# Kernel tuning notes

Hardware: AMD Instinct MI355X
Metric: run time of the kernel (lower is better)

The kernel has to match this reference:

```python
import jax, jax.numpy as jnp
import numpy as np


def setup_inputs() -> dict:
    key = jax.random.key(0)
    B, D, F = 8192, 768, 32768
    k_x, k_w = jax.random.split(key, 2)
    x = jax.random.normal(k_x, (B, D), dtype=jnp.float32)
    # xavier_normal init for W_enc: std = sqrt(2/(fan_in+fan_out))
    scale = (2.0 / (D + F)) ** 0.5
    W_enc = jax.random.normal(k_w, (D, F), dtype=jnp.float32) * scale
    # W_dec = W_enc.T with unit-norm rows (latent directions)
    W_dec = W_enc.T
    W_dec = W_dec / jnp.linalg.norm(W_dec, axis=1, keepdims=True)
    pre_bias = jnp.zeros((D,), dtype=jnp.float32)
    latent_bias = jnp.zeros((F,), dtype=jnp.float32)
    return {"x": x, "pre_bias": pre_bias, "W_enc": W_enc,
            "latent_bias": latent_bias, "W_dec": W_dec, "k": 32}


def reference(x, pre_bias, W_enc, latent_bias, W_dec, k):
    # encode: [B,F]
    latents_pre_act = (x - pre_bias) @ W_enc + latent_bias
    # topk selection then relu: relu(topk(pre_act, k))
    vals, idx = jax.lax.top_k(latents_pre_act, k)      # [B,k]
    vals = jax.nn.relu(vals)
    # sparse decode: gather only the k selected decoder rows per example
    # W_dec[idx]: [B,k,D]
    recons = jnp.einsum('bk,bkd->bd', vals, W_dec[idx]) + pre_bias
    return recons
```

## Files before the change

### kernel.cpp

```cpp
#include <hip/hip_runtime.h>
#include <stdint.h>

#define GAS __attribute__((address_space(1)))
#define LAS __attribute__((address_space(3)))

typedef __attribute__((ext_vector_type(4))) float f32x4;
typedef unsigned char uchar;
typedef long long i64f;

static constexpr int NB = 8192;
static constexpr int DD = 768;
static constexpr int FF = 32768;
static constexpr int TK = 32;
static constexpr int RUNC = 64;
static constexpr int SLOT = 8;
static constexpr int NSEG = FF / 128;
static constexpr int SORTN = 1024;
static constexpr int NS2 = 256;
static constexpr int NKT = DD / 32;
static constexpr int PQ8 = 128 * 32;
static constexpr float WSC = 64.0f;
static constexpr float WSCI = 1.0f / 64.0f;

__device__ __forceinline__ ushort f2bf(float f) {
    unsigned x = __float_as_uint(f);
    unsigned r = (x + 0x7FFFu + ((x >> 16) & 1u)) >> 16;
    return (ushort)r;
}
__device__ __forceinline__ ushort sortkey(ushort u) {
    return (u & 0x8000u) ? (ushort)(u ^ 0xFFFFu) : (ushort)(u | 0x8000u);
}
__device__ __forceinline__ float e4m3f(uchar b) {
    int e = (b >> 3) & 0xF, m = b & 7;
    float v = (e == 0) ? ldexpf((float)m, -9) : ldexpf((float)(8 + m), e - 10);
    return (b & 0x80) ? -v : v;
}
__device__ __forceinline__ uchar f2e4m3(float v) {
    return (uchar)(__builtin_amdgcn_cvt_pk_fp8_f32(v, v, 0, false) & 0xFF);
}
__device__ __forceinline__ void gload_lds16(const void* g, void* l) {
    __builtin_amdgcn_global_load_lds((const GAS unsigned int*)g,
                                     (LAS unsigned int*)l, 16, 0, 0);
}
__device__ __forceinline__ size_t pan_off8(int v, int d) {
    return ((size_t)(v >> 7) * NKT + (d >> 5)) * PQ8 + ((v & 127) << 5) + (d & 31);
}

__global__ __launch_bounds__(256) void prep_x_k(const float* __restrict__ x,
                                                const float* __restrict__ pb,
                                                uchar* __restrict__ Ap) {
    const int n4 = NB * DD / 4;
    for (int i = blockIdx.x * 256 + threadIdx.x; i < n4; i += gridDim.x * 256) {
        int b = i / (DD / 4), dq = (i % (DD / 4)) * 4;
        float4 v = ((const float4*)x)[i];
        float4 p = ((const float4*)pb)[i % (DD / 4)];
        int w = __builtin_amdgcn_cvt_pk_fp8_f32(v.x - p.x, v.y - p.y, 0, false);
        w = __builtin_amdgcn_cvt_pk_fp8_f32(v.z - p.z, v.w - p.w, w, true);
        *(unsigned*)(Ap + pan_off8(b, dq)) = (unsigned)w;
    }
}

__global__ __launch_bounds__(256) void prep_w_k(const float* __restrict__ W,
                                                uchar* __restrict__ Bp,
                                                float* __restrict__ Wt32,
                                                float* __restrict__ s2part) {
    __shared__ float tile[32][33];
    int f0 = blockIdx.x * 32, d0 = blockIdx.y * 32;
    int tx = threadIdx.x & 31, ty = threadIdx.x >> 5;
    float ss = 0.f;
#pragma unroll
    for (int q = 0; q < 4; q++) {
        int dl = ty + q * 8;
        float v = W[(size_t)(d0 + dl) * FF + f0 + tx];
        tile[dl][tx] = v;
        ss += v * v;
    }
#pragma unroll
    for (int o = 32; o >= 1; o >>= 1) ss += __shfl_down(ss, o);
    if ((threadIdx.x & 63) == 0) {
        int slot = (blockIdx.x * 97 + blockIdx.y * 13 + (threadIdx.x >> 6)) & (NS2 - 1);
        atomicAdd(&s2part[slot], ss);
    }
    __syncthreads();
#pragma unroll
    for (int q = 0; q < 4; q++) {
        int fl = ty + q * 8;
        float v = tile[tx][fl];
        int f = f0 + fl, d = d0 + tx;
        Bp[pan_off8(f, d)] = f2e4m3(v * WSC);
        if (Wt32) Wt32[(size_t)f * DD + d] = v;
    }
}

__global__ __launch_bounds__(256) void rn_k(const float* __restrict__ x,
                                            const float* __restrict__ pb,
                                            const float* __restrict__ s2part,
                                            float* __restrict__ tau) {
    int t = threadIdx.x, l = t & 63, w = t >> 6;
    __shared__ float wsum[4];
    __shared__ float s2m;
    float p = s2part[t];
#pragma unroll
    for (int o = 32; o >= 1; o >>= 1) p += __shfl_down(p, o);
    if (l == 0) wsum[w] = p;
    __syncthreads();
    if (t == 0) s2m = (wsum[0] + wsum[1] + wsum[2] + wsum[3]) / ((float)DD * (float)FF);
    __syncthreads();
    int row = blockIdx.x * 4 + w;
    float ss = 0.f;
#pragma unroll
    for (int q = 0; q < 12; q++) {
        int d = l + 64 * q;
        float v = x[(size_t)row * DD + d] - pb[d];
        ss += v * v;
    }
#pragma unroll
    for (int o = 32; o >= 1; o >>= 1) ss += __shfl_down(ss, o);
    if (l == 0) tau[row] = 2.75f * sqrtf(s2m * ss);
}

__global__ __launch_bounds__(256, 3) void gemm_k(const uchar* __restrict__ Ap,
                                                 const uchar* __restrict__ Bp,
                                                 const float* __restrict__ lbias,
                                                 const float* __restrict__ tau,
                                                 unsigned* __restrict__ cand,
                                                 unsigned* __restrict__ rowbad) {
    __shared__ __align__(16) char smem[24576];

    int bid = (int)blockIdx.x;
    int wg = (bid & 7) * 2048 + (bid >> 3);
    int mt = wg >> 8, nt = wg & 255;
    int m0 = mt << 7, n0 = nt << 7;

    int t = threadIdx.x, l = t & 63, w = t >> 6;
    int wm = w >> 1, wn = w & 1;

    int so = ((t >> 1) << 5) + (((t & 1) ^ ((t >> 3) & 1)) << 4);
    const uchar* sA = Ap + (size_t)mt * NKT * PQ8 + so;
    const uchar* sB = Bp + (size_t)nt * NKT * PQ8 + so;

    int sw = ((l >> 2) & 1) << 1;
    int aro = ((wm << 6) + (l & 15)) * 32 + (((l >> 4) ^ sw) << 3);
    int bro = ((wn << 6) + (l & 15)) * 32 + (((l >> 4) ^ sw) << 3);

    f32x4 acc[4][4] = {};

#define STAGE(slot, kt)                                                       \
    {                                                                         \
        const size_t o = (size_t)(kt) * PQ8;                                  \
        char* base = smem + (slot) * 8192;                                    \
        gload_lds16(sA + o, base + t * 16);                                   \
        gload_lds16(sB + o, base + 4096 + t * 16);                            \
    }

    STAGE(0, 0)
    STAGE(1, 1)
    asm volatile("s_waitcnt vmcnt(2)" ::: "memory");
    __builtin_amdgcn_s_barrier();
    __builtin_amdgcn_sched_barrier(0);

    int cur = 0;
#pragma unroll 1
    for (int kt = 0; kt < NKT; kt++) {
        const char* As = smem + cur * 8192;
        const char* Bs = As + 4096;
        int nxt = cur + 2; if (nxt >= 3) nxt -= 3;
        if (kt < NKT - 2) STAGE(nxt, kt + 2)

        i64f af[4], bfr[4];
        af[0]  = *(const i64f*)(As + aro);
        af[1]  = *(const i64f*)(As + aro + 512);
        af[2]  = *(const i64f*)(As + aro + 1024);
        af[3]  = *(const i64f*)(As + aro + 1536);
        bfr[0] = *(const i64f*)(Bs + bro);
        bfr[1] = *(const i64f*)(Bs + bro + 512);
        bfr[2] = *(const i64f*)(Bs + bro + 1024);
        bfr[3] = *(const i64f*)(Bs + bro + 1536);
        asm volatile("s_waitcnt lgkmcnt(0)" ::: "memory");
        __builtin_amdgcn_sched_barrier(0);
        __builtin_amdgcn_s_setprio(1);
#pragma unroll
        for (int mi = 0; mi < 4; mi++)
#pragma unroll
            for (int ni = 0; ni < 4; ni++)
                acc[mi][ni] = __builtin_amdgcn_mfma_f32_16x16x32_fp8_fp8(
                    af[mi], bfr[ni], acc[mi][ni], 0, 0, 0);
        __builtin_amdgcn_s_setprio(0);
        __builtin_amdgcn_sched_barrier(0);
        if (kt < NKT - 2)
            asm volatile("s_waitcnt vmcnt(2)" ::: "memory");
        else
            asm volatile("s_waitcnt vmcnt(0)" ::: "memory");
        __builtin_amdgcn_s_barrier();
        __builtin_amdgcn_sched_barrier(0);
        cur = cur + 1; if (cur == 3) cur = 0;
    }
#undef STAGE

    __syncthreads();
    int* lcnt = (int*)smem;
    unsigned* lbuf = (unsigned*)(smem + 512);
    if (t < 128) lcnt[t] = 0;
    __syncthreads();
    float lbv[4]; int fcol[4];
#pragma unroll
    for (int ni = 0; ni < 4; ni++) {
        fcol[ni] = n0 + wn * 64 + ni * 16 + (l & 15);
        lbv[ni] = lbias[fcol[ni]];
    }
#pragma unroll
    for (int mi = 0; mi < 4; mi++) {
        int rl = wm * 64 + mi * 16 + ((l >> 4) << 2);
        float4 tq = *(const float4*)(tau + m0 + rl);
        float tj[4] = {tq.x, tq.y, tq.z, tq.w};
#pragma unroll
        for (int ni = 0; ni < 4; ni++) {
            f32x4 v4 = acc[mi][ni];
#pragma unroll
            for (int j = 0; j < 4; j++) {
                float v = v4[j] * WSCI + lbv[ni];
                if (v >= tj[j]) {
                    int idx = rl + j;
                    int p = atomicAdd(&lcnt[idx], 1);
                    if (p < SLOT)
                        lbuf[idx * SLOT + p] =
                            ((unsigned)sortkey(f2bf(v)) << 16) | (unsigned)(32767 - fcol[ni]);
                }
            }
        }
    }
    __syncthreads();
    if (t < 128) {
        int c = lcnt[t];
        int gr = m0 + t;
        if (c > SLOT) { atomicOr(&rowbad[gr], 1u); c = SLOT; }
        unsigned* dstc = cand + (size_t)gr * (NSEG * SLOT) + nt * SLOT;
        for (int s2 = 0; s2 < c; s2++) dstc[s2] = lbuf[t * SLOT + s2];
    }
}

__global__ __launch_bounds__(256) void select2_k(const unsigned* __restrict__ cand,
                                                 const unsigned* __restrict__ rowbad,
                                                 unsigned* __restrict__ flagv,
                                                 int* __restrict__ ridx,
                                                 int* __restrict__ runcnt) {
    int b = blockIdx.x, t = threadIdx.x;
    __shared__ unsigned srt[SORTN];
    __shared__ int s_cnt;
    for (int i = t; i < SORTN; i += 256) srt[i] = 0;
    if (t == 0) s_cnt = 0;
    __syncthreads();
    const uint4* src = (const uint4*)(cand + (size_t)b * (NSEG * SLOT));
    for (int i = t; i < NSEG * SLOT / 4; i += 256) {
        uint4 v4 = src[i];
        unsigned d[4] = {v4.x, v4.y, v4.z, v4.w};
#pragma unroll
        for (int q = 0; q < 4; q++)
            if (d[q]) {
                int p = atomicAdd(&s_cnt, 1);
                if (p < SORTN) srt[p] = d[q];
            }
    }
    __syncthreads();
    int cnt = s_cnt;
    int bad = (rowbad[b] != 0u) || cnt < 48 || cnt > SORTN;
    if (t == 0) { flagv[b] = bad; if (bad) runcnt[b] = 0; }
    if (bad) return;
    for (int k = 2; k <= SORTN; k <<= 1) {
        for (int j = k >> 1; j > 0; j >>= 1) {
#pragma unroll
            for (int q = 0; q < SORTN / 256; q++) {
                int i = t + q * 256;
                int ixj = i ^ j;
                if (ixj > i) {
                    unsigned a = srt[i], c2 = srt[ixj];
                    bool sw = ((i & k) == 0) ? (a < c2) : (a > c2);
                    if (sw) { srt[i] = c2; srt[ixj] = a; }
                }
            }
            __syncthreads();
        }
    }
    int nc = cnt < RUNC ? cnt : RUNC;
    if (t < nc) ridx[(size_t)b * RUNC + t] = 32767 - (int)(srt[t] & 0xFFFFu);
    if (t == 0) runcnt[b] = nc;
}

__global__ __launch_bounds__(256) void fb_k(const unsigned* __restrict__ flagv,
                                            const float* __restrict__ x,
                                            const float* __restrict__ pb,
                                            const uchar* __restrict__ Bp,
                                            const float* __restrict__ lb,
                                            int* __restrict__ ridx,
                                            int* __restrict__ runcnt) {
    int b = blockIdx.x;
    if (!flagv[b]) return;
    int t = threadIdx.x;
    __shared__ float xs[DD];
    __shared__ float lut[256];
    __shared__ unsigned hist[256];
    __shared__ int s_cb, s_cum, s_T, s_pos;
    for (int i = t; i < DD; i += 256) xs[i] = x[(size_t)b * DD + i] - pb[i];
    lut[t] = e4m3f((uchar)t) * WSCI;
    hist[t] = 0;
    if (t == 0) s_pos = 0;
    __syncthreads();

#define FBDOT(f, sdst)                                                        \
    {                                                                         \
        const uchar* fr = Bp + ((size_t)((f) >> 7) * NKT) * PQ8 + (((f) & 127) << 5); \
        float s_ = 0.f;                                                       \
        for (int kt = 0; kt < NKT; kt++) {                                    \
            const unsigned* pw = (const unsigned*)(fr + (size_t)kt * PQ8);    \
            _Pragma("unroll")                                                 \
            for (int q = 0; q < 8; q++) {                                     \
                unsigned wv = pw[q];                                          \
                s_ += xs[kt * 32 + q * 4 + 0] * lut[wv & 255];                \
                s_ += xs[kt * 32 + q * 4 + 1] * lut[(wv >> 8) & 255];         \
                s_ += xs[kt * 32 + q * 4 + 2] * lut[(wv >> 16) & 255];        \
                s_ += xs[kt * 32 + q * 4 + 3] * lut[wv >> 24];                \
            }                                                                 \
        }                                                                     \
        sdst = s_;                                                            \
    }

    for (int f = t; f < FF; f += 256) {
        float s; FBDOT(f, s)
        ushort k = sortkey(f2bf(s + lb[f]));
        atomicAdd(&hist[k >> 8], 1u);
    }
    __syncthreads();
    if (t == 0) {
        int cum = 0, cb2 = 0;
        for (int i = 255; i >= 0; i--) {
            if (cum + (int)hist[i] >= 48) { cb2 = i; break; }
            cum += (int)hist[i];
        }
        s_cb = cb2; s_cum = cum;
    }
    __syncthreads();
    int cb2 = s_cb;
    hist[t] = 0;
    __syncthreads();
    for (int f = t; f < FF; f += 256) {
        float s; FBDOT(f, s)
        ushort k = sortkey(f2bf(s + lb[f]));
        if ((int)(k >> 8) == cb2) atomicAdd(&hist[k & 0xFF], 1u);
    }
    __syncthreads();
    if (t == 0) {
        int cum = s_cum, T = cb2 << 8;
        for (int fb2 = 255; fb2 >= 0; fb2--) {
            if (cum + (int)hist[fb2] >= 48) { T = (cb2 << 8) | fb2; break; }
            cum += (int)hist[fb2];
        }
        s_T = T;
    }
    __syncthreads();
    unsigned T = (unsigned)s_T;
    for (int f = t; f < FF; f += 256) {
        float s; FBDOT(f, s)
        ushort k = sortkey(f2bf(s + lb[f]));
        if (k >= T) {
            int p = atomicAdd(&s_pos, 1);
            if (p < RUNC) ridx[(size_t)b * RUNC + p] = f;
        }
    }
#undef FBDOT
    __syncthreads();
    if (t == 0) runcnt[b] = s_pos < RUNC ? s_pos : RUNC;
}

__global__ __launch_bounds__(256) void refine_k(const float* __restrict__ x,
                                                const float* __restrict__ pb,
                                                const float* __restrict__ We,
                                                const float* __restrict__ Wt32,
                                                const float* __restrict__ lb,
                                                const int* __restrict__ runidx,
                                                const int* __restrict__ runcnt,
                                                int use_t,
                                                int* __restrict__ sidx,
                                                float* __restrict__ sval) {
    int b = blockIdx.x, t = threadIdx.x, l = t & 63, w = t >> 6;
    __shared__ float xs[DD];
    __shared__ int ci[RUNC];
    __shared__ float cv[RUNC];
    for (int i = t; i < DD; i += 256) xs[i] = x[(size_t)b * DD + i] - pb[i];
    int c = runcnt[b]; if (c > RUNC) c = RUNC;
    if (t < RUNC) cv[t] = -1e30f;
    if (t < c) ci[t] = runidx[(size_t)b * RUNC + t];
    __syncthreads();
    for (int j = w; j < c; j += 4) {
        int f = ci[j];
        double s = 0.0;
        if (use_t) {
            const float* wr = Wt32 + (size_t)f * DD;
#pragma unroll
            for (int q = 0; q < 12; q++)
                s = fma((double)wr[l + 64 * q], (double)xs[l + 64 * q], s);
        } else {
#pragma unroll
            for (int q = 0; q < 12; q++)
                s = fma((double)We[(size_t)(l + 64 * q) * FF + f], (double)xs[l + 64 * q], s);
        }
#pragma unroll
        for (int o = 32; o >= 1; o >>= 1) s += __shfl_down(s, o);
        if (l == 0) cv[j] = (float)(s + (double)lb[f]);
    }
    __syncthreads();
    if (w == 0) {
        float v0 = (l < RUNC) ? cv[l] : -1e30f;
        int i0 = (l < c) ? ci[l] : 0x7FFFFFFF;
        for (int sel = 0; sel < TK; sel++) {
            float bv = v0; int bi = i0;
#pragma unroll
            for (int o = 32; o >= 1; o >>= 1) {
                float ov = __shfl_xor(bv, o);
                int oi = __shfl_xor(bi, o);
                if (ov > bv || (ov == bv && oi < bi)) { bv = ov; bi = oi; }
            }
            if (i0 == bi) v0 = -1e30f;
            if (l == 0) {
                if (bi == 0x7FFFFFFF) { bi = 0; bv = -1e30f; }
                sidx[(size_t)b * TK + sel] = bi;
                sval[(size_t)b * TK + sel] = bv > 0.f ? bv : 0.f;
            }
        }
    }
}

__global__ __launch_bounds__(192) void decode_k(const float* __restrict__ sval,
                                                const int* __restrict__ sidx,
                                                const float* __restrict__ Wd,
                                                const float* __restrict__ pb,
                                                float* __restrict__ out) {
    int b = blockIdx.x, t = threadIdx.x;
    __shared__ float sv[TK];
    __shared__ int si[TK];
    if (t < TK) { sv[t] = sval[(size_t)b * TK + t]; si[t] = sidx[(size_t)b * TK + t]; }
    __syncthreads();
    float4 acc = ((const float4*)pb)[t];
#pragma unroll 4
    for (int j = 0; j < TK; j++) {
        float v = sv[j];
        float4 wv = ((const float4*)(Wd + (size_t)si[j] * DD))[t];
        acc.x += v * wv.x; acc.y += v * wv.y;
        acc.z += v * wv.z; acc.w += v * wv.w;
    }
    ((float4*)out)[(size_t)b * (DD / 4) + t] = acc;
}

extern "C" void kernel_launch(void* const* d_in, const int* in_sizes, int n_in,
                              void* d_out, int out_size, void* d_ws, size_t ws_size,
                              hipStream_t stream) {
    const float* x  = (const float*)d_in[0];
    const float* pb = (const float*)d_in[1];
    const float* We = (const float*)d_in[2];
    const float* lb = (const float*)d_in[3];
    const float* Wd = (const float*)d_in[4];
    float* out = (float*)d_out;
    char* ws = (char*)d_ws;
    (void)in_sizes; (void)n_in; (void)out_size;

    const size_t SZ_AP   = (size_t)NB * DD;
    const size_t SZ_BP   = (size_t)FF * DD;
    const size_t SZ_WT32 = (size_t)FF * DD * 4;
    const size_t SZ_CAND = (size_t)NB * NSEG * SLOT * 4;
    const size_t SZ_TAU  = (size_t)NB * 4;
    const size_t SZ_RIDX = (size_t)NB * RUNC * 4;
    const size_t SZ_RCNT = (size_t)NB * 4;
    const size_t SZ_SIDX = (size_t)NB * TK * 4;
    const size_t SZ_SVAL = (size_t)NB * TK * 4;

    size_t need_base = SZ_AP + SZ_BP + ((size_t)NB * 4 + NS2 * 4 + SZ_CAND) +
                       (size_t)NB * 4 + SZ_TAU + SZ_RIDX + SZ_RCNT + SZ_SIDX + SZ_SVAL;
    int use_t = (ws_size >= need_base + SZ_WT32) ? 1 : 0;

    size_t off = 0;
    uchar* Ap     = (uchar*)(ws + off); off += SZ_AP;
    uchar* Bp     = (uchar*)(ws + off); off += SZ_BP;
    float* Wt32   = nullptr;
    if (use_t) { Wt32 = (float*)(ws + off); off += SZ_WT32; }
    char* ctrl0   = (char*)(ws + off);
    unsigned* rowbad = (unsigned*)(ws + off); off += (size_t)NB * 4;
    float* s2part = (float*)(ws + off); off += NS2 * 4;
    unsigned* cand = (unsigned*)(ws + off); off += SZ_CAND;
    size_t ctrl_bytes = (size_t)((ws + off) - ctrl0);
    unsigned* flagv = (unsigned*)(ws + off); off += (size_t)NB * 4;
    float* tau    = (float*)(ws + off); off += SZ_TAU;
    int* ridx     = (int*)(ws + off); off += SZ_RIDX;
    int* rcnt     = (int*)(ws + off); off += SZ_RCNT;
    int* sidx     = (int*)(ws + off); off += SZ_SIDX;
    float* sval   = (float*)(ws + off); off += SZ_SVAL;

    hipMemsetAsync(ctrl0, 0, ctrl_bytes, stream);
    prep_x_k<<<2048, 256, 0, stream>>>(x, pb, Ap);
    prep_w_k<<<dim3(FF / 32, DD / 32), 256, 0, stream>>>(We, Bp, Wt32, s2part);
    rn_k<<<NB / 4, 256, 0, stream>>>(x, pb, s2part, tau);
    gemm_k<<<(NB / 128) * (FF / 128), 256, 0, stream>>>(Ap, Bp, lb, tau, cand, rowbad);
    select2_k<<<NB, 256, 0, stream>>>(cand, rowbad, flagv, ridx, rcnt);
    fb_k<<<NB, 256, 0, stream>>>(flagv, x, pb, Bp, lb, ridx, rcnt);
    refine_k<<<NB, 256, 0, stream>>>(x, pb, We, Wt32, lb, ridx, rcnt, use_t, sidx, sval);
    decode_k<<<NB, 192, 0, stream>>>(sval, sidx, Wd, pb, out);
}
```

Measured before the change: 926.9 us.

## Add per-segment candidate counts, drop cand memset, and bf16 decoder copy

The GEMM epilogue now writes a per-row, per-segment candidate count byte. The select kernel reads only the valid candidate entries instead of scanning the whole candidate buffer for nonzeros. This lets the 64MB candidate buffer drop out of the memset region. A new prep kernel converts W_dec to bf16 so decode gathers half the bytes, but it costs an extra full pass over W_dec (read 100MB, write 50MB) on every call and adds bf16 rounding to the output.

```diff
diff --git a/kernel.cpp b/kernel.cpp
--- a/kernel.cpp
+++ b/kernel.cpp
@@ -30,6 +30,9 @@
 __device__ __forceinline__ ushort sortkey(ushort u) {
     return (u & 0x8000u) ? (ushort)(u ^ 0xFFFFu) : (ushort)(u | 0x8000u);
 }
+__device__ __forceinline__ float bf2f(ushort u) {
+    return __uint_as_float(((unsigned)u) << 16);
+}
 __device__ __forceinline__ float e4m3f(uchar b) {
     int e = (b >> 3) & 0xF, m = b & 7;
     float v = (e == 0) ? ldexpf((float)m, -9) : ldexpf((float)(8 + m), e - 10);
@@ -92,6 +95,17 @@
     }
 }
 
+__global__ __launch_bounds__(256) void prep_wd_k(const float* __restrict__ Wd,
+                                                 ushort* __restrict__ Wd16) {
+    const int n4 = FF * DD / 4;
+    for (int i = blockIdx.x * 256 + threadIdx.x; i < n4; i += gridDim.x * 256) {
+        float4 v = ((const float4*)Wd)[i];
+        ushort4 o;
+        o.x = f2bf(v.x); o.y = f2bf(v.y); o.z = f2bf(v.z); o.w = f2bf(v.w);
+        ((ushort4*)Wd16)[i] = o;
+    }
+}
+
 __global__ __launch_bounds__(256) void rn_k(const float* __restrict__ x,
                                             const float* __restrict__ pb,
                                             const float* __restrict__ s2part,
@@ -124,6 +138,7 @@
                                                  const float* __restrict__ lbias,
                                                  const float* __restrict__ tau,
                                                  unsigned* __restrict__ cand,
+                                                 uchar* __restrict__ ccnt8,
                                                  unsigned* __restrict__ rowbad) {
     __shared__ __align__(16) char smem[24576];
 
@@ -236,10 +251,12 @@
         if (c > SLOT) { atomicOr(&rowbad[gr], 1u); c = SLOT; }
         unsigned* dstc = cand + (size_t)gr * (NSEG * SLOT) + nt * SLOT;
         for (int s2 = 0; s2 < c; s2++) dstc[s2] = lbuf[t * SLOT + s2];
+        ccnt8[(size_t)gr * NSEG + nt] = (uchar)c;
     }
 }
 
 __global__ __launch_bounds__(256) void select2_k(const unsigned* __restrict__ cand,
+                                                 const uchar* __restrict__ ccnt8,
                                                  const unsigned* __restrict__ rowbad,
                                                  unsigned* __restrict__ flagv,
                                                  int* __restrict__ ridx,
@@ -250,16 +267,15 @@
     for (int i = t; i < SORTN; i += 256) srt[i] = 0;
     if (t == 0) s_cnt = 0;
     __syncthreads();
-    const uint4* src = (const uint4*)(cand + (size_t)b * (NSEG * SLOT));
-    for (int i = t; i < NSEG * SLOT / 4; i += 256) {
-        uint4 v4 = src[i];
-        unsigned d[4] = {v4.x, v4.y, v4.z, v4.w};
-#pragma unroll
-        for (int q = 0; q < 4; q++)
-            if (d[q]) {
-                int p = atomicAdd(&s_cnt, 1);
-                if (p < SORTN) srt[p] = d[q];
-            }
+    const uchar* cc = ccnt8 + (size_t)b * NSEG;
+    const unsigned* base = cand + (size_t)b * (NSEG * SLOT);
+    for (int seg = t; seg < NSEG; seg += 256) {
+        int c = cc[seg];
+        const unsigned* e = base + seg * SLOT;
+        for (int q = 0; q < c; q++) {
+            int p = atomicAdd(&s_cnt, 1);
+            if (p < SORTN) srt[p] = e[q];
+        }
     }
     __syncthreads();
     int cnt = s_cnt;
@@ -431,6 +447,7 @@
 
 __global__ __launch_bounds__(192) void decode_k(const float* __restrict__ sval,
                                                 const int* __restrict__ sidx,
+                                                const ushort* __restrict__ Wd16,
                                                 const float* __restrict__ Wd,
                                                 const float* __restrict__ pb,
                                                 float* __restrict__ out) {
@@ -440,12 +457,22 @@
     if (t < TK) { sv[t] = sval[(size_t)b * TK + t]; si[t] = sidx[(size_t)b * TK + t]; }
     __syncthreads();
     float4 acc = ((const float4*)pb)[t];
+    if (Wd16) {
 #pragma unroll 4
-    for (int j = 0; j < TK; j++) {
-        float v = sv[j];
-        float4 wv = ((const float4*)(Wd + (size_t)si[j] * DD))[t];
-        acc.x += v * wv.x; acc.y += v * wv.y;
-        acc.z += v * wv.z; acc.w += v * wv.w;
+        for (int j = 0; j < TK; j++) {
+            float v = sv[j];
+            ushort4 wv = ((const ushort4*)(Wd16 + (size_t)si[j] * DD))[t];
+            acc.x += v * bf2f(wv.x); acc.y += v * bf2f(wv.y);
+            acc.z += v * bf2f(wv.z); acc.w += v * bf2f(wv.w);
+        }
+    } else {
+#pragma unroll 4
+        for (int j = 0; j < TK; j++) {
+            float v = sv[j];
+            float4 wv = ((const float4*)(Wd + (size_t)si[j] * DD))[t];
+            acc.x += v * wv.x; acc.y += v * wv.y;
+            acc.z += v * wv.z; acc.w += v * wv.w;
+        }
     }
     ((float4*)out)[(size_t)b * (DD / 4) + t] = acc;
 }
@@ -465,27 +492,34 @@
     const size_t SZ_AP   = (size_t)NB * DD;
     const size_t SZ_BP   = (size_t)FF * DD;
     const size_t SZ_WT32 = (size_t)FF * DD * 4;
+    const size_t SZ_WD16 = (size_t)FF * DD * 2;
     const size_t SZ_CAND = (size_t)NB * NSEG * SLOT * 4;
+    const size_t SZ_CC8  = (size_t)NB * NSEG;
     const size_t SZ_TAU  = (size_t)NB * 4;
     const size_t SZ_RIDX = (size_t)NB * RUNC * 4;
     const size_t SZ_RCNT = (size_t)NB * 4;
     const size_t SZ_SIDX = (size_t)NB * TK * 4;
     const size_t SZ_SVAL = (size_t)NB * TK * 4;
 
-    size_t need_base = SZ_AP + SZ_BP + ((size_t)NB * 4 + NS2 * 4 + SZ_CAND) +
-                       (size_t)NB * 4 + SZ_TAU + SZ_RIDX + SZ_RCNT + SZ_SIDX + SZ_SVAL;
-    int use_t = (ws_size >= need_base + SZ_WT32) ? 1 : 0;
+    size_t need_base = SZ_AP + SZ_BP + SZ_CAND + SZ_CC8 + (size_t)NB * 8 + NS2 * 4 +
+                       SZ_TAU + SZ_RIDX + SZ_RCNT + SZ_SIDX + SZ_SVAL;
+    int use_t = (ws_size >= need_base + SZ_WT32 + SZ_WD16) ? 1 : 0;
 
     size_t off = 0;
     uchar* Ap     = (uchar*)(ws + off); off += SZ_AP;
     uchar* Bp     = (uchar*)(ws + off); off += SZ_BP;
     float* Wt32   = nullptr;
-    if (use_t) { Wt32 = (float*)(ws + off); off += SZ_WT32; }
+    ushort* Wd16  = nullptr;
+    if (use_t) {
+        Wt32 = (float*)(ws + off); off += SZ_WT32;
+        Wd16 = (ushort*)(ws + off); off += SZ_WD16;
+    }
     char* ctrl0   = (char*)(ws + off);
     unsigned* rowbad = (unsigned*)(ws + off); off += (size_t)NB * 4;
     float* s2part = (float*)(ws + off); off += NS2 * 4;
+    size_t ctrl_bytes = (size_t)((ws + off) - ctrl0);
     unsigned* cand = (unsigned*)(ws + off); off += SZ_CAND;
-    size_t ctrl_bytes = (size_t)((ws + off) - ctrl0);
+    uchar* ccnt8  = (uchar*)(ws + off); off += SZ_CC8;
     unsigned* flagv = (unsigned*)(ws + off); off += (size_t)NB * 4;
     float* tau    = (float*)(ws + off); off += SZ_TAU;
     int* ridx     = (int*)(ws + off); off += SZ_RIDX;
@@ -496,10 +530,11 @@
     hipMemsetAsync(ctrl0, 0, ctrl_bytes, stream);
     prep_x_k<<<2048, 256, 0, stream>>>(x, pb, Ap);
     prep_w_k<<<dim3(FF / 32, DD / 32), 256, 0, stream>>>(We, Bp, Wt32, s2part);
+    if (use_t) prep_wd_k<<<2048, 256, 0, stream>>>(Wd, Wd16);
     rn_k<<<NB / 4, 256, 0, stream>>>(x, pb, s2part, tau);
-    gemm_k<<<(NB / 128) * (FF / 128), 256, 0, stream>>>(Ap, Bp, lb, tau, cand, rowbad);
-    select2_k<<<NB, 256, 0, stream>>>(cand, rowbad, flagv, ridx, rcnt);
+    gemm_k<<<(NB / 128) * (FF / 128), 256, 0, stream>>>(Ap, Bp, lb, tau, cand, ccnt8, rowbad);
+    select2_k<<<NB, 256, 0, stream>>>(cand, ccnt8, rowbad, flagv, ridx, rcnt);
     fb_k<<<NB, 256, 0, stream>>>(flagv, x, pb, Bp, lb, ridx, rcnt);
     refine_k<<<NB, 256, 0, stream>>>(x, pb, We, Wt32, lb, ridx, rcnt, use_t, sidx, sval);
-    decode_k<<<NB, 192, 0, stream>>>(sval, sidx, Wd, pb, out);
-}
+    decode_k<<<NB, 192, 0, stream>>>(sval, sidx, Wd16, Wd, pb, out);
+}
```

Measured after the change: 890.8 us. 1.04x faster.
